# Kernel tuning notes

Hardware: AMD Instinct MI355X
Metric: run time of the kernel (lower is better)

The kernel has to match this reference:

```python
import jax, jax.numpy as jnp
import numpy as np

B, S, DIM, LW, CHUNK = 4, 4096, 512, 512, 64


def _l2n(x):
    n = jnp.sqrt(jnp.sum(x * x, axis=-1, keepdims=True))
    return x / jnp.maximum(n, 1e-12)


def setup_inputs() -> dict:
    key = jax.random.key(0)
    k = jax.random.split(key, 10)
    s = 1.0 / np.sqrt(DIM)
    return {
        "x": jax.random.normal(k[0], (B, S, DIM), jnp.float32),
        "Wq": jax.random.normal(k[1], (DIM, DIM), jnp.float32) * s,
        "Wk": jax.random.normal(k[2], (DIM, DIM), jnp.float32) * s,
        "Wv": jax.random.normal(k[3], (DIM, DIM), jnp.float32) * s,
        "init_w1": jax.random.normal(k[4], (LW, DIM), jnp.float32) * 0.02,
        "init_b1": jnp.zeros((LW,), jnp.float32),
        "init_w2": jax.random.normal(k[5], (DIM, LW), jnp.float32) * 0.02,
        "init_b2": jnp.zeros((DIM,), jnp.float32),
        "alpha_w": jax.random.normal(k[6], (DIM,), jnp.float32) * s,
        "alpha_b": jnp.full((1,), -5.0, jnp.float32),
        "eta_w": jax.random.normal(k[7], (DIM,), jnp.float32) * s,
        "eta_b": jnp.full((1,), 2.0, jnp.float32),
        "theta_w": jax.random.normal(k[8], (DIM,), jnp.float32) * s,
        "theta_b": jnp.full((1,), -4.6, jnp.float32),
        "chunk_size": CHUNK,
    }


def reference(x, Wq, Wk, Wv, init_w1, init_b1, init_w2, init_b2,
              alpha_w, alpha_b, eta_w, eta_b, theta_w, theta_b, chunk_size):
    b, s, d = x.shape
    c = int(chunk_size)
    nC = s // c
    lw = init_w1.shape[0]
    # per-sample memory params (broadcast of shared init) + zero momentum
    w1 = jnp.broadcast_to(init_w1, (b, lw, d))
    b1 = jnp.broadcast_to(init_b1, (b, lw))
    w2 = jnp.broadcast_to(init_w2, (b, d, lw))
    b2 = jnp.broadcast_to(init_b2, (b, d))
    mom = (jnp.zeros_like(w1), jnp.zeros_like(b1), jnp.zeros_like(w2), jnp.zeros_like(b2))
    xc = x.reshape(b, nC, c, d).transpose(1, 0, 2, 3)  # [nC, B, C, D]

    def step(carry, x_c):
        (w1, b1, w2, b2), (mw1, mb1, mw2, mb2) = carry
        q = _l2n(x_c @ Wq.T)
        k_ = _l2n(x_c @ Wk.T)
        v = x_c @ Wv.T
        # gates per token -> chunk-averaged, [B]
        a = jax.nn.sigmoid(x_c @ alpha_w + alpha_b).mean(axis=1)
        e = jax.nn.sigmoid(x_c @ eta_w + eta_b).mean(axis=1)
        t = jax.nn.sigmoid(x_c @ theta_w + theta_b).mean(axis=1)
        # retrieval with stale (chunk-constant) memory params
        hq = jax.nn.silu(jnp.einsum('bcd,bhd->bch', q, w1) + b1[:, None, :])
        y = jnp.einsum('bch,bdh->bcd', hq, w2) + b2[:, None, :]
        # per-token grads of mse(mlp(k), v) (mean over feature dim), chunk-averaged.
        # Analytic grads == autodiff of the tiny MLP; avoids [B,C,LW,D] intermediates.
        pre = jnp.einsum('bcd,bhd->bch', k_, w1) + b1[:, None, :]
        sg = jax.nn.sigmoid(pre)
        hk = pre * sg  # silu
        vp = jnp.einsum('bch,bdh->bcd', hk, w2) + b2[:, None, :]
        dvp = 2.0 * (vp - v) / d  # dL/d vp for mse over feature dim
        g_b2 = dvp.mean(axis=1)
        g_w2 = jnp.einsum('bcd,bch->bdh', dvp, hk) / c
        dh = jnp.einsum('bcd,bdh->bch', dvp, w2) * (sg * (1.0 + pre * (1.0 - sg)))
        g_b1 = dh.mean(axis=1)
        g_w1 = jnp.einsum('bch,bcd->bhd', dh, k_) / c
        a3, e3, t3 = a[:, None, None], e[:, None, None], t[:, None, None]
        a2, e2, t2 = a[:, None], e[:, None], t[:, None]
        nmw1 = e3 * mw1 - t3 * g_w1
        nmb1 = e2 * mb1 - t2 * g_b1
        nmw2 = e3 * mw2 - t3 * g_w2
        nmb2 = e2 * mb2 - t2 * g_b2
        nw1 = (1.0 - a3) * w1 + nmw1
        nb1 = (1.0 - a2) * b1 + nmb1
        nw2 = (1.0 - a3) * w2 + nmw2
        nb2 = (1.0 - a2) * b2 + nmb2
        return ((nw1, nb1, nw2, nb2), (nmw1, nmb1, nmw2, nmb2)), y

    _, ys = jax.lax.scan(step, ((w1, b1, w2, b2), mom), xc)
    return ys.transpose(1, 0, 2, 3).reshape(b, s, d)
```

## Files before the change

### kernel.cpp

```cpp
#include <hip/hip_runtime.h>
#include <hip/hip_bf16.h>

#define BB 4
#define SS 4096
#define DD 512
#define LWW 512
#define CC 64
#define NCH 64

typedef unsigned short u16;
using fragAB = __attribute__((ext_vector_type(8))) short;
using fragC  = __attribute__((ext_vector_type(4))) float;
using u16x4  = __attribute__((ext_vector_type(4))) short;

__device__ __forceinline__ short f2bf(float f){
  unsigned u = __float_as_uint(f);
  u = (u + 0x7FFFu + ((u >> 16) & 1u)) >> 16;
  return (short)u;
}
__device__ __forceinline__ float bf2f(short s){
  return __uint_as_float(((unsigned)(u16)s) << 16);
}
__device__ __forceinline__ fragC zeroC(){ fragC z = {0.f,0.f,0.f,0.f}; return z; }

__device__ __forceinline__ fragAB frag_bf16g(const u16* __restrict__ base, int ld, int r0, int k0, int lane){
  return *(const fragAB*)(base + (size_t)(r0 + (lane & 15)) * ld + k0 + ((lane >> 4) << 3));
}
__device__ __forceinline__ fragAB frag_lds(const short* base, int ld, int r0, int k0, int lane){
  return *(const fragAB*)(base + (r0 + (lane & 15)) * ld + k0 + ((lane >> 4) << 3));
}
#define MFMA16(a,b,c) __builtin_amdgcn_mfma_f32_16x16x32_bf16(a,b,c,0,0,0)

__device__ __forceinline__ void ld_sys(fragAB& r, const u16* p){
  asm volatile("global_load_dwordx4 %0, %1, off sc0 sc1" : "=v"(r) : "v"(p) : "memory");
}
__device__ __forceinline__ void st_sys8(u16* p, u16x4 v){
  asm volatile("global_store_dwordx2 %0, %1, off sc0 sc1" :: "v"(p), "v"(v) : "memory");
}
__device__ __forceinline__ void st_sys16(u16* p, fragAB v){
  asm volatile("global_store_dwordx4 %0, %1, off sc0 sc1" :: "v"(p), "v"(v) : "memory");
}
#define WAITVM(N) do { asm volatile("s_waitcnt vmcnt(" #N ")" ::: "memory"); \
                       __builtin_amdgcn_sched_barrier(0); } while (0)

__device__ __forceinline__ const u16* taddr(const u16* base, int c, int kq){
  return base + (((size_t)((kq >> 4)*64 + c)) << 4) + (kq & 15);
}

__device__ __forceinline__ void bar_sync(unsigned* slots, unsigned phase, int tl){
  asm volatile("s_waitcnt vmcnt(0)" ::: "memory");
  __builtin_amdgcn_sched_barrier(0);
  __syncthreads();
  if (threadIdx.x == 0)
    __hip_atomic_store(slots + (size_t)tl*32, phase, __ATOMIC_RELAXED, __HIP_MEMORY_SCOPE_AGENT);
  if (threadIdx.x < 64){
    bool mine = threadIdx.x < 32;
    unsigned* sp = slots + (size_t)(threadIdx.x & 31)*32;
    for (;;){
      unsigned v = mine ? __hip_atomic_load(sp, __ATOMIC_RELAXED, __HIP_MEMORY_SCOPE_AGENT) : phase;
      if (__all((int)(v >= phase))) break;
      __builtin_amdgcn_s_sleep(1);
    }
  }
  __syncthreads();
}

__global__ __launch_bounds__(256) void k_cvt(const float* __restrict__ x,
    const float* __restrict__ Wq, const float* __restrict__ Wk, const float* __restrict__ Wv,
    u16* __restrict__ xb, u16* __restrict__ Wc, unsigned* __restrict__ bar){
  size_t i = (size_t)blockIdx.x * 256 + threadIdx.x;
  if (blockIdx.x == 0){
    for (int z = threadIdx.x; z < 4096; z += 256) bar[z] = 0u;
  }
  const size_t NX4 = (size_t)BB*SS*DD/4;
  const size_t NW4 = (size_t)DD*DD/4;
  if (i < NX4){
    float4 v = ((const float4*)x)[i];
    u16x4 o = { f2bf(v.x), f2bf(v.y), f2bf(v.z), f2bf(v.w) };
    *(u16x4*)(xb + 4*i) = o;
  } else if (i < NX4 + 3*NW4){
    size_t j = i - NX4;
    const float* src = (j < NW4) ? Wq : (j < 2*NW4) ? Wk : Wv;
    size_t jj = j % NW4;
    float4 v = ((const float4*)src)[jj];
    u16x4 o = { f2bf(v.x), f2bf(v.y), f2bf(v.z), f2bf(v.w) };
    *(u16x4*)(Wc + 4*j) = o;
  }
}

__global__ __launch_bounds__(256) void k_proj(const u16* __restrict__ xb,
    const u16* __restrict__ Wc,
    u16* __restrict__ Qb, u16* __restrict__ Kb, float* __restrict__ V){
  int mt = blockIdx.x / 12, nt = blockIdx.x % 12;
  int lane = threadIdx.x & 63, wid = threadIdx.x >> 6;
  int m0 = mt * 64 + wid * 16;
  const u16* Bp = Wc + (size_t)nt * 128 * DD;
  fragC acc[8];
#pragma unroll
  for (int i = 0; i < 8; ++i) acc[i] = zeroC();
  for (int k0 = 0; k0 < DD; k0 += 32){
    fragAB a = frag_bf16g(xb, DD, m0, k0, lane);
#pragma unroll
    for (int nf = 0; nf < 8; ++nf)
      acc[nf] = MFMA16(a, frag_bf16g(Bp, DD, nf*16, k0, lane), acc[nf]);
  }
#pragma unroll
  for (int nf = 0; nf < 8; ++nf){
#pragma unroll
    for (int r = 0; r < 4; ++r){
      int m = m0 + ((lane >> 4) << 2) + r;
      int col = nt*128 + nf*16 + (lane & 15);
      float v = acc[nf][r];
      if (nt < 4)      Qb[(size_t)m*DD + col]        = (u16)f2bf(v);
      else if (nt < 8) Kb[(size_t)m*DD + col - 512]  = (u16)f2bf(v);
      else             V [(size_t)m*DD + col - 1024] = v;
    }
  }
}

__global__ __launch_bounds__(256) void k_norm(u16* __restrict__ Qb, u16* __restrict__ Kb){
  int idx = blockIdx.x * 4 + (threadIdx.x >> 6);
  int lane = threadIdx.x & 63;
  u16* p = (idx < BB*SS ? Qb + (size_t)idx * DD
                        : Kb + (size_t)(idx - BB*SS) * DD) + lane * 8;
  fragAB v = *(const fragAB*)p;
  float f[8]; float s = 0.f;
#pragma unroll
  for (int i = 0; i < 8; ++i){ f[i] = bf2f(v[i]); s += f[i]*f[i]; }
#pragma unroll
  for (int o = 32; o > 0; o >>= 1) s += __shfl_xor(s, o, 64);
  float inv = 1.f / fmaxf(sqrtf(s), 1e-12f);
  fragAB o8;
#pragma unroll
  for (int i = 0; i < 8; ++i) o8[i] = f2bf(f[i] * inv);
  *(fragAB*)p = o8;
}

__global__ __launch_bounds__(256) void k_trans(const u16* __restrict__ Kb, u16* __restrict__ KT){
  __shared__ short tile[64][68];
  int blk = blockIdx.x;
  int b = blk >> 9, rem = blk & 511;
  int st = rem >> 3, dt = rem & 7;
  int s0 = st*64, d0 = dt*64;
  int sr = threadIdx.x & 63, q = threadIdx.x >> 6;
  const u16* src = Kb + ((size_t)b*SS + s0 + sr)*DD + d0 + q*16;
  fragAB v0 = *(const fragAB*)src;
  fragAB v1 = *(const fragAB*)(src + 8);
#pragma unroll
  for (int i = 0; i < 8; ++i){ tile[sr][q*16+i] = v0[i]; tile[sr][q*16+8+i] = v1[i]; }
  __syncthreads();
  fragAB o0, o1;
#pragma unroll
  for (int i = 0; i < 8; ++i){ o0[i] = tile[q*16+i][sr]; o1[i] = tile[q*16+8+i][sr]; }
  u16* dst = KT + ((size_t)b*DD + d0 + sr)*SS + s0 + q*16;
  *(fragAB*)dst = o0;
  *(fragAB*)(dst + 8) = o1;
}

__global__ __launch_bounds__(256) void k_gates(const float* __restrict__ x,
    const float* __restrict__ aw, const float* __restrict__ ab,
    const float* __restrict__ ew, const float* __restrict__ eb,
    const float* __restrict__ tw, const float* __restrict__ tb,
    float* __restrict__ aet){
  __shared__ float part[64][4][3];
  __shared__ float rowsig[64][3];
  int b = blockIdx.x >> 6, t = blockIdx.x & 63;
  int tid = threadIdx.x;
  int r = tid >> 2, p = tid & 3;
  const float4* xp = (const float4*)(x + ((size_t)b*SS + (size_t)t*CC + r) * DD + p * 128);
  const float4* a4 = (const float4*)(aw + p*128);
  const float4* e4 = (const float4*)(ew + p*128);
  const float4* t4 = (const float4*)(tw + p*128);
  float s0 = 0.f, s1 = 0.f, s2 = 0.f;
  for (int i = 0; i < 32; ++i){
    float4 xv = xp[i], av = a4[i], ev = e4[i], tv = t4[i];
    s0 += xv.x*av.x + xv.y*av.y + xv.z*av.z + xv.w*av.w;
    s1 += xv.x*ev.x + xv.y*ev.y + xv.z*ev.z + xv.w*ev.w;
    s2 += xv.x*tv.x + xv.y*tv.y + xv.z*tv.z + xv.w*tv.w;
  }
  part[r][p][0] = s0; part[r][p][1] = s1; part[r][p][2] = s2;
  __syncthreads();
  if (tid < 64){
    float a_ = part[tid][0][0]+part[tid][1][0]+part[tid][2][0]+part[tid][3][0] + ab[0];
    float e_ = part[tid][0][1]+part[tid][1][1]+part[tid][2][1]+part[tid][3][1] + eb[0];
    float t_ = part[tid][0][2]+part[tid][1][2]+part[tid][2][2]+part[tid][3][2] + tb[0];
    rowsig[tid][0] = 1.f/(1.f+expf(-a_));
    rowsig[tid][1] = 1.f/(1.f+expf(-e_));
    rowsig[tid][2] = 1.f/(1.f+expf(-t_));
  }
  __syncthreads();
  if (tid < 3){
    float s = 0.f;
    for (int i = 0; i < 64; ++i) s += rowsig[i][tid];
    aet[((size_t)b*NCH + t)*3 + tid] = s * (1.f/64.f);
  }
}

__global__ __launch_bounds__(512, 2) void k_scan(
    const u16* __restrict__ Qb, const u16* __restrict__ Kb, const u16* __restrict__ KTg,
    const float* __restrict__ V, const float* __restrict__ aet,
    const float* __restrict__ iw1, const float* __restrict__ ib1,
    const float* __restrict__ iw2, const float* __restrict__ ib2,
    u16* __restrict__ hkb, u16* __restrict__ hqs, u16* __restrict__ hkT,
    u16* __restrict__ dvpb, u16* __restrict__ w2Tb,
    float* __restrict__ out, unsigned* __restrict__ barb)
{
  __shared__ __align__(16) short s_w1[16*520];
  __shared__ __align__(16) short s_w2[16*520];
  __shared__ __align__(16) short s_pf[16*520];
  __shared__ __align__(16) short s_t[16*72];
  __shared__ __align__(16) short s_hk[64*16];
  __shared__ __align__(16) short s_hq[64*16];
  __shared__ float s_part[64][17];
  __shared__ float s_b1[16], s_mb1[16], s_b2[16], s_mb2[16];

  const int tid  = threadIdx.x;
  const int lane = tid & 63;
  const int wid  = tid >> 6;
  const int q    = lane >> 4;
  const int l15  = lane & 15;
  const int qk   = q << 3;
  const int b    = (blockIdx.x & 7) >> 1;
  const int tl   = ((blockIdx.x >> 3) << 1) | (blockIdx.x & 1);
  const int h0   = tl * 16;
  const int d0   = tl * 16;
  unsigned* slots = barb + (size_t)b * 1024;
  unsigned  ph   = 0;

  const u16* Kball = Kb  + (size_t)b*SS*DD;
  const u16* Qball = Qb  + (size_t)b*SS*DD;
  const u16* KTbat = KTg + (size_t)b*DD*SS;
  u16* hk_b  = hkb  + (size_t)b*CC*LWW;
  u16* hq_b  = hqs  + (size_t)b*CC*LWW;
  u16* hkT_b = hkT  + (size_t)b*LWW*CC;
  u16* dv_b  = dvpb + (size_t)b*CC*DD;
  const size_t W2TBUF = (size_t)BB*DD*LWW;

  float w1f[16], mw1f[16], w2f[16], mw2f[16], actr[4];

  {
    u16* w2T0 = w2Tb + (size_t)b*DD*LWW;
#pragma unroll
    for (int nf = 0; nf < 4; ++nf){
      u16x4 pk;
#pragma unroll
      for (int r = 0; r < 4; ++r){
        int hr = q*4 + r;
        int dcol = wid*64 + nf*16 + l15;
        float a = iw1[(size_t)(h0 + hr)*DD + dcol];
        w1f[nf*4+r] = a; mw1f[nf*4+r] = 0.f;
        s_w1[hr*520 + dcol] = f2bf(a);
        float c = iw2[(size_t)(d0 + hr)*LWW + dcol];
        w2f[nf*4+r] = c; mw2f[nf*4+r] = 0.f;
        s_w2[hr*520 + dcol] = f2bf(c);
        pk[r] = f2bf(c);
      }
      st_sys8(w2T0 + (size_t)(wid*64 + nf*16 + l15)*DD + d0 + q*4, pk);
    }
    if (tid < 16){
      s_b1[tid] = ib1[h0 + tid]; s_mb1[tid] = 0.f;
      s_b2[tid] = ib2[d0 + tid]; s_mb2[tid] = 0.f;
    }
#pragma unroll
    for (int r = 0; r < 4; ++r) actr[r] = 0.f;
    WAITVM(0);
    __syncthreads();
  }

  for (int t = 0; t < NCH; ++t){
    if (t > 0){
      fragAB kfr[8];
      {
        const u16* KTm = KTbat + (size_t)(t-1)*CC;
#pragma unroll
        for (int nf = 0; nf < 4; ++nf)
#pragma unroll
          for (int kk = 0; kk < 2; ++kk)
            kfr[nf*2+kk] = frag_bf16g(KTm, SS, wid*64 + nf*16, kk*32, lane);
      }
      {
        const int cst = (wid & 3) * 16;
        const int kh  = (wid >> 2) * 256;
        fragAB fa[8];
        fragC a0 = zeroC();
#pragma unroll
        for (int j = 0; j < 8; ++j) ld_sys(fa[j], taddr(dv_b, cst + l15, kh + j*32 + qk));
        WAITVM(4);
#pragma unroll
        for (int j = 0; j < 4; ++j) a0 = MFMA16(fa[j], frag_lds(s_pf, 520, 0, kh + j*32, lane), a0);
        WAITVM(0);
#pragma unroll
        for (int j = 4; j < 8; ++j) a0 = MFMA16(fa[j], frag_lds(s_pf, 520, 0, kh + j*32, lane), a0);
        if (wid >= 4){
#pragma unroll
          for (int r = 0; r < 4; ++r) s_part[cst + q*4 + r][l15] = a0[r];
        }
        __syncthreads();
        if (wid < 4){
#pragma unroll
          for (int r = 0; r < 4; ++r){
            float v = (a0[r] + s_part[cst + q*4 + r][l15]) * actr[r];
            s_t[l15*72 + cst + q*4 + r] = f2bf(v);
          }
        }
      }
      __syncthreads();
      {
        fragC ag[4];
#pragma unroll
        for (int i = 0; i < 4; ++i) ag[i] = zeroC();
#pragma unroll
        for (int kk = 0; kk < 2; ++kk){
          fragAB af = frag_lds(s_t, 72, 0, kk*32, lane);
#pragma unroll
          for (int nf = 0; nf < 4; ++nf)
            ag[nf] = MFMA16(af, kfr[nf*2+kk], ag[nf]);
        }
        const float* g3 = aet + ((size_t)b*NCH + (t-1)) * 3;
        float ga = g3[0], ge = g3[1], gth = g3[2];
#pragma unroll
        for (int nf = 0; nf < 4; ++nf)
#pragma unroll
          for (int r = 0; r < 4; ++r){
            float g  = ag[nf][r] * (1.f/64.f);
            float m_ = ge*mw1f[nf*4+r] - gth*g;
            float w_ = (1.f-ga)*w1f[nf*4+r] + m_;
            mw1f[nf*4+r] = m_; w1f[nf*4+r] = w_;
            s_w1[(q*4+r)*520 + wid*64 + nf*16 + l15] = f2bf(w_);
          }
        if (tid < 16){
          const fragAB* row = (const fragAB*)(s_t + tid*72);
          float s = 0.f;
#pragma unroll
          for (int j = 0; j < 8; ++j){
            fragAB v = row[j];
#pragma unroll
            for (int i = 0; i < 8; ++i) s += bf2f(v[i]);
          }
          float gb = s * (1.f/64.f);
          float m_ = ge*s_mb1[tid] - gth*gb;
          float bn = (1.f-ga)*s_b1[tid] + m_;
          s_mb1[tid] = m_; s_b1[tid] = bn;
        }
      }
    }
    __syncthreads();
    {
      const u16* Ac = (wid < 4 ? Kball : Qball) + (size_t)t*CC*DD;
      int m0 = (wid & 3) * 16;
      fragC acc = zeroC();
      for (int k0 = 0; k0 < DD; k0 += 32)
        acc = MFMA16(frag_bf16g(Ac, DD, m0, k0, lane),
                     frag_lds(s_w1, 520, 0, k0, lane), acc);
      float bb = s_b1[l15];
      if (wid < 4){
        u16x4 pk;
#pragma unroll
        for (int r = 0; r < 4; ++r){
          int c = m0 + q*4 + r;
          float pre = acc[r] + bb;
          float sg  = 1.f/(1.f+expf(-pre));
          float hkv = pre * sg;
          actr[r]   = sg * (1.f + pre * (1.f - sg));
          short hb  = f2bf(hkv);
          s_hk[c*16 + l15] = hb;
          pk[r] = hb;
        }
        st_sys8(hkT_b + (size_t)(h0 + l15)*CC + m0 + q*4, pk);
      } else {
#pragma unroll
        for (int r = 0; r < 4; ++r){
          int c = m0 + q*4 + r;
          float hqv = acc[r] + bb;
          float s2  = 1.f/(1.f+expf(-hqv));
          s_hq[c*16 + l15] = f2bf(hqv * s2);
        }
      }
    }
    __syncthreads();
    if (tid < 128){
      st_sys16(hk_b + (size_t)tl*1024 + tid*8, *(const fragAB*)(s_hk + tid*8));
    } else if (tid < 256){
      int i = tid - 128;
      st_sys16(hq_b + (size_t)tl*1024 + i*8, *(const fragAB*)(s_hq + i*8));
    }
    ph++; bar_sync(slots, ph, tl);

    {
      const u16* Ah = (wid < 4) ? hq_b : hk_b;
      int m0 = (wid & 3) * 16;
      fragC acc = zeroC();
      fragAB va[4], vb[4], hfr[8];
      float vv[4];
      if (wid >= 4){
#pragma unroll
        for (int r = 0; r < 4; ++r)
          vv[r] = V[((size_t)b*SS + (size_t)t*CC + m0 + q*4 + r)*DD + d0 + l15];
      }
#pragma unroll
      for (int j = 0; j < 4; ++j) ld_sys(va[j], taddr(Ah, m0 + l15, j*32 + qk));
#pragma unroll
      for (int j = 0; j < 4; ++j) ld_sys(vb[j], taddr(Ah, m0 + l15, 128 + j*32 + qk));
      WAITVM(4);
#pragma unroll
      for (int j = 0; j < 4; ++j) acc = MFMA16(va[j], frag_lds(s_w2, 520, 0, j*32, lane), acc);
#pragma unroll
      for (int j = 0; j < 4; ++j) ld_sys(va[j], taddr(Ah, m0 + l15, 256 + j*32 + qk));
      WAITVM(4);
#pragma unroll
      for (int j = 0; j < 4; ++j) acc = MFMA16(vb[j], frag_lds(s_w2, 520, 0, 128 + j*32, lane), acc);
#pragma unroll
      for (int j = 0; j < 4; ++j) ld_sys(vb[j], taddr(Ah, m0 + l15, 384 + j*32 + qk));
      WAITVM(4);
#pragma unroll
      for (int j = 0; j < 4; ++j) acc = MFMA16(va[j], frag_lds(s_w2, 520, 0, 256 + j*32, lane), acc);
#pragma unroll
      for (int nf = 0; nf < 4; ++nf)
#pragma unroll
        for (int kk = 0; kk < 2; ++kk)
          ld_sys(hfr[nf*2+kk], hkT_b + (size_t)(wid*64 + nf*16 + l15)*CC + kk*32 + qk);
      WAITVM(8);
#pragma unroll
      for (int j = 0; j < 4; ++j) acc = MFMA16(vb[j], frag_lds(s_w2, 520, 0, 384 + j*32, lane), acc);

      float bb = s_b2[l15];
      if (wid < 4){
#pragma unroll
        for (int r = 0; r < 4; ++r){
          int c = m0 + q*4 + r;
          __builtin_nontemporal_store(acc[r] + bb,
            &out[((size_t)b*SS + (size_t)t*CC + c)*DD + d0 + l15]);
        }
      } else {
#pragma unroll
        for (int r = 0; r < 4; ++r){
          int c = m0 + q*4 + r;
          float dvv = (acc[r] + bb - vv[r]) * (2.f/512.f);
          short db_ = f2bf(dvv);
          s_hk[c*16 + l15] = db_;
          s_t[l15*72 + c]  = db_;
        }
      }
      __syncthreads();
      if (wid < 4) { WAITVM(4); } else { WAITVM(0); }
      if (tid < 128)
        st_sys16(dv_b + (size_t)tl*1024 + tid*8, *(const fragAB*)(s_hk + tid*8));
      {
        fragC ag[4];
#pragma unroll
        for (int i = 0; i < 4; ++i) ag[i] = zeroC();
#pragma unroll
        for (int kk = 0; kk < 2; ++kk){
          fragAB af = frag_lds(s_t, 72, 0, kk*32, lane);
#pragma unroll
          for (int nf = 0; nf < 4; ++nf)
            ag[nf] = MFMA16(af, hfr[nf*2+kk], ag[nf]);
        }
        fragAB t0, t1;
        int hr = tid >> 5;
        int c0 = (tid & 31) << 4;
        if (t + 1 < NCH){
          const u16* w2Tp = w2Tb + (size_t)(t&1)*W2TBUF + (size_t)b*DD*LWW;
          const u16* src = w2Tp + (size_t)(h0 + hr)*DD + c0;
          ld_sys(t0, src);
          ld_sys(t1, src + 8);
        }
        const float* g3 = aet + ((size_t)b*NCH + t) * 3;
        float ga = g3[0], ge = g3[1], gth = g3[2];
        u16* w2Tn = w2Tb + (size_t)((t+1)&1)*W2TBUF + (size_t)b*DD*LWW;
#pragma unroll
        for (int nf = 0; nf < 4; ++nf){
          u16x4 pk;
#pragma unroll
          for (int r = 0; r < 4; ++r){
            float g  = ag[nf][r] * (1.f/64.f);
            float m_ = ge*mw2f[nf*4+r] - gth*g;
            float w_ = (1.f-ga)*w2f[nf*4+r] + m_;
            mw2f[nf*4+r] = m_; w2f[nf*4+r] = w_;
            short wb = f2bf(w_);
            s_w2[(q*4+r)*520 + wid*64 + nf*16 + l15] = wb;
            pk[r] = wb;
          }
          st_sys8(w2Tn + (size_t)(wid*64 + nf*16 + l15)*DD + d0 + q*4, pk);
        }
        if (tid < 16){
          const fragAB* row = (const fragAB*)(s_t + tid*72);
          float s = 0.f;
#pragma unroll
          for (int j = 0; j < 8; ++j){
            fragAB v = row[j];
#pragma unroll
            for (int i = 0; i < 8; ++i) s += bf2f(v[i]);
          }
          float gb = s * (1.f/64.f);
          float m_ = ge*s_mb2[tid] - gth*gb;
          float bn = (1.f-ga)*s_b2[tid] + m_;
          s_mb2[tid] = m_; s_b2[tid] = bn;
        }
        if (t + 1 < NCH){
          WAITVM(0);
          *(fragAB*)(s_pf + hr*520 + c0)     = t0;
          *(fragAB*)(s_pf + hr*520 + c0 + 8) = t1;
        }
      }
    }
    ph++; bar_sync(slots, ph, tl);
  }
}

extern "C" void kernel_launch(void* const* d_in, const int* in_sizes, int n_in,
                              void* d_out, int out_size, void* d_ws, size_t ws_size,
                              hipStream_t stream){
  const float* x   = (const float*)d_in[0];
  const float* Wq  = (const float*)d_in[1];
  const float* Wk  = (const float*)d_in[2];
  const float* Wv  = (const float*)d_in[3];
  const float* iw1 = (const float*)d_in[4];
  const float* ib1 = (const float*)d_in[5];
  const float* iw2 = (const float*)d_in[6];
  const float* ib2 = (const float*)d_in[7];
  const float* aw  = (const float*)d_in[8];
  const float* ab  = (const float*)d_in[9];
  const float* ew  = (const float*)d_in[10];
  const float* eb  = (const float*)d_in[11];
  const float* tw  = (const float*)d_in[12];
  const float* tb  = (const float*)d_in[13];
  float* out = (float*)d_out;

  float* fw = (float*)d_ws;
  float* V    = fw;  fw += (size_t)BB*SS*DD;
  float* aet  = fw;  fw += (size_t)BB*NCH*3 + 64;
  unsigned* bar = (unsigned*)fw; fw += 4096;
  u16* xb   = (u16*)fw;
  u16* Wc   = xb   + (size_t)BB*SS*DD;
  u16* Qb   = Wc   + (size_t)3*DD*DD;
  u16* Kb   = Qb   + (size_t)BB*SS*DD;
  u16* hkb  = Kb   + (size_t)BB*SS*DD;
  u16* hqs  = hkb  + (size_t)BB*CC*LWW;
  u16* hkT  = hqs  + (size_t)BB*CC*LWW;
  u16* dvpb = hkT  + (size_t)BB*LWW*CC;
  u16* w2Tb = dvpb + (size_t)BB*CC*DD;
  u16* KTg  = xb;

  k_cvt  <<<8960, 256, 0, stream>>>(x, Wq, Wk, Wv, xb, Wc, bar);
  k_proj <<<3072, 256, 0, stream>>>(xb, Wc, Qb, Kb, V);
  k_norm <<<8192, 256, 0, stream>>>(Qb, Kb);
  k_trans<<<2048, 256, 0, stream>>>(Kb, KTg);
  k_gates<<<256,  256, 0, stream>>>(x, aw, ab, ew, eb, tw, tb, aet);
  k_scan <<<128,  512, 0, stream>>>(Qb, Kb, KTg, V, aet, iw1, ib1, iw2, ib2,
                                    hkb, hqs, hkT, dvpb, w2Tb, out, bar);
}
```

Measured before the change: 1.438 ms.

## Replace transposed w2 exchange with redundant column-slice w2 update and split barriers

Each block now keeps its own transposed column slice of w2 in registers and LDS, and updates it locally from an exchanged transposed dvp and a locally stored hk transpose. This replaces writing the full transposed w2 to global memory and reloading it every chunk. The grid barrier is split into arrive and wait halves so the redundant w2c update overlaps barrier latency. The cost is extra MFMA work, registers and LDS per block, plus extra dvT global stores.

Measured after the change: 1.756 ms. 1.22x slower.

```diff
diff --git a/kernel.cpp b/kernel.cpp
--- a/kernel.cpp
+++ b/kernel.cpp
@@ -47,12 +47,14 @@
   return base + (((size_t)((kq >> 4)*64 + c)) << 4) + (kq & 15);
 }
 
-__device__ __forceinline__ void bar_sync(unsigned* slots, unsigned phase, int tl){
+__device__ __forceinline__ void bar_arrive(unsigned* slots, unsigned phase, int tl){
   asm volatile("s_waitcnt vmcnt(0)" ::: "memory");
   __builtin_amdgcn_sched_barrier(0);
   __syncthreads();
   if (threadIdx.x == 0)
     __hip_atomic_store(slots + (size_t)tl*32, phase, __ATOMIC_RELAXED, __HIP_MEMORY_SCOPE_AGENT);
+}
+__device__ __forceinline__ void bar_wait(unsigned* slots, unsigned phase){
   if (threadIdx.x < 64){
     bool mine = threadIdx.x < 32;
     unsigned* sp = slots + (size_t)(threadIdx.x & 31)*32;
@@ -202,13 +204,14 @@
     const float* __restrict__ iw1, const float* __restrict__ ib1,
     const float* __restrict__ iw2, const float* __restrict__ ib2,
     u16* __restrict__ hkb, u16* __restrict__ hqs, u16* __restrict__ hkT,
-    u16* __restrict__ dvpb, u16* __restrict__ w2Tb,
+    u16* __restrict__ dvpb, u16* __restrict__ dvTg,
     float* __restrict__ out, unsigned* __restrict__ barb)
 {
   __shared__ __align__(16) short s_w1[16*520];
   __shared__ __align__(16) short s_w2[16*520];
-  __shared__ __align__(16) short s_pf[16*520];
+  __shared__ __align__(16) short s_w2c[16*520];
   __shared__ __align__(16) short s_t[16*72];
+  __shared__ __align__(16) short s_hkTb[2][16*72];
   __shared__ __align__(16) short s_hk[64*16];
   __shared__ __align__(16) short s_hq[64*16];
   __shared__ float s_part[64][17];
@@ -234,15 +237,13 @@
   u16* hq_b  = hqs  + (size_t)b*CC*LWW;
   u16* hkT_b = hkT  + (size_t)b*LWW*CC;
   u16* dv_b  = dvpb + (size_t)b*CC*DD;
-  const size_t W2TBUF = (size_t)BB*DD*LWW;
-
-  float w1f[16], mw1f[16], w2f[16], mw2f[16], actr[4];
+  u16* dvT_b = dvTg + (size_t)b*DD*CC;
+
+  float w1f[16], mw1f[16], w2f[16], mw2f[16], w2cf[16], mw2cf[16], actr[4];
 
   {
-    u16* w2T0 = w2Tb + (size_t)b*DD*LWW;
 #pragma unroll
     for (int nf = 0; nf < 4; ++nf){
-      u16x4 pk;
 #pragma unroll
       for (int r = 0; r < 4; ++r){
         int hr = q*4 + r;
@@ -253,9 +254,10 @@
         float c = iw2[(size_t)(d0 + hr)*LWW + dcol];
         w2f[nf*4+r] = c; mw2f[nf*4+r] = 0.f;
         s_w2[hr*520 + dcol] = f2bf(c);
-        pk[r] = f2bf(c);
-      }
-      st_sys8(w2T0 + (size_t)(wid*64 + nf*16 + l15)*DD + d0 + q*4, pk);
+        float c2 = iw2[(size_t)dcol*LWW + (h0 + hr)];
+        w2cf[nf*4+r] = c2; mw2cf[nf*4+r] = 0.f;
+        s_w2c[hr*520 + dcol] = f2bf(c2);
+      }
     }
     if (tid < 16){
       s_b1[tid] = ib1[h0 + tid]; s_mb1[tid] = 0.f;
@@ -263,11 +265,11 @@
     }
 #pragma unroll
     for (int r = 0; r < 4; ++r) actr[r] = 0.f;
-    WAITVM(0);
     __syncthreads();
   }
 
   for (int t = 0; t < NCH; ++t){
+    fragAB dfr[8];
     if (t > 0){
       fragAB kfr[8];
       {
@@ -287,10 +289,10 @@
         for (int j = 0; j < 8; ++j) ld_sys(fa[j], taddr(dv_b, cst + l15, kh + j*32 + qk));
         WAITVM(4);
 #pragma unroll
-        for (int j = 0; j < 4; ++j) a0 = MFMA16(fa[j], frag_lds(s_pf, 520, 0, kh + j*32, lane), a0);
+        for (int j = 0; j < 4; ++j) a0 = MFMA16(fa[j], frag_lds(s_w2c, 520, 0, kh + j*32, lane), a0);
         WAITVM(0);
 #pragma unroll
-        for (int j = 4; j < 8; ++j) a0 = MFMA16(fa[j], frag_lds(s_pf, 520, 0, kh + j*32, lane), a0);
+        for (int j = 4; j < 8; ++j) a0 = MFMA16(fa[j], frag_lds(s_w2c, 520, 0, kh + j*32, lane), a0);
         if (wid >= 4){
 #pragma unroll
           for (int r = 0; r < 4; ++r) s_part[cst + q*4 + r][l15] = a0[r];
@@ -355,6 +357,7 @@
       float bb = s_b1[l15];
       if (wid < 4){
         u16x4 pk;
+        short* hT = &s_hkTb[t & 1][0];
 #pragma unroll
         for (int r = 0; r < 4; ++r){
           int c = m0 + q*4 + r;
@@ -364,6 +367,7 @@
           actr[r]   = sg * (1.f + pre * (1.f - sg));
           short hb  = f2bf(hkv);
           s_hk[c*16 + l15] = hb;
+          hT[l15*72 + c]   = hb;
           pk[r] = hb;
         }
         st_sys8(hkT_b + (size_t)(h0 + l15)*CC + m0 + q*4, pk);
@@ -384,7 +388,40 @@
       int i = tid - 128;
       st_sys16(hq_b + (size_t)tl*1024 + i*8, *(const fragAB*)(s_hq + i*8));
     }
-    ph++; bar_sync(slots, ph, tl);
+    if (t > 0){
+#pragma unroll
+      for (int nf = 0; nf < 4; ++nf)
+#pragma unroll
+        for (int kk = 0; kk < 2; ++kk)
+          ld_sys(dfr[nf*2+kk], dvT_b + (size_t)(wid*64 + nf*16 + l15)*CC + kk*32 + qk);
+    }
+    ph++; bar_arrive(slots, ph, tl);
+    if (t > 0){
+      fragC ag2[4];
+#pragma unroll
+      for (int i = 0; i < 4; ++i) ag2[i] = zeroC();
+      const short* hTp = &s_hkTb[(t-1) & 1][0];
+#pragma unroll
+      for (int kk = 0; kk < 2; ++kk){
+        fragAB af2 = frag_lds(hTp, 72, 0, kk*32, lane);
+#pragma unroll
+        for (int nf = 0; nf < 4; ++nf)
+          ag2[nf] = MFMA16(af2, dfr[nf*2+kk], ag2[nf]);
+      }
+      const float* g3 = aet + ((size_t)b*NCH + (t-1)) * 3;
+      float ga = g3[0], ge = g3[1], gth = g3[2];
+#pragma unroll
+      for (int nf = 0; nf < 4; ++nf)
+#pragma unroll
+        for (int r = 0; r < 4; ++r){
+          float g  = ag2[nf][r] * (1.f/64.f);
+          float m_ = ge*mw2cf[nf*4+r] - gth*g;
+          float w_ = (1.f-ga)*w2cf[nf*4+r] + m_;
+          mw2cf[nf*4+r] = m_; w2cf[nf*4+r] = w_;
+          s_w2c[(q*4+r)*520 + wid*64 + nf*16 + l15] = f2bf(w_);
+        }
+    }
+    bar_wait(slots, ph);
 
     {
       const u16* Ah = (wid < 4) ? hq_b : hk_b;
@@ -442,9 +479,14 @@
         }
       }
       __syncthreads();
-      if (wid < 4) { WAITVM(4); } else { WAITVM(0); }
-      if (tid < 128)
+      if (tid < 128){
         st_sys16(dv_b + (size_t)tl*1024 + tid*8, *(const fragAB*)(s_hk + tid*8));
+      } else if (tid < 256){
+        int i = tid - 128;
+        int row = i >> 3, seg = i & 7;
+        st_sys16(dvT_b + (size_t)(d0 + row)*CC + seg*8, *(const fragAB*)(s_t + row*72 + seg*8));
+      }
+      ph++; bar_arrive(slots, ph, tl);
       {
         fragC ag[4];
 #pragma unroll
@@ -456,33 +498,18 @@
           for (int nf = 0; nf < 4; ++nf)
             ag[nf] = MFMA16(af, hfr[nf*2+kk], ag[nf]);
         }
-        fragAB t0, t1;
-        int hr = tid >> 5;
-        int c0 = (tid & 31) << 4;
-        if (t + 1 < NCH){
-          const u16* w2Tp = w2Tb + (size_t)(t&1)*W2TBUF + (size_t)b*DD*LWW;
-          const u16* src = w2Tp + (size_t)(h0 + hr)*DD + c0;
-          ld_sys(t0, src);
-          ld_sys(t1, src + 8);
-        }
         const float* g3 = aet + ((size_t)b*NCH + t) * 3;
         float ga = g3[0], ge = g3[1], gth = g3[2];
-        u16* w2Tn = w2Tb + (size_t)((t+1)&1)*W2TBUF + (size_t)b*DD*LWW;
-#pragma unroll
-        for (int nf = 0; nf < 4; ++nf){
-          u16x4 pk;
+#pragma unroll
+        for (int nf = 0; nf < 4; ++nf)
 #pragma unroll
           for (int r = 0; r < 4; ++r){
             float g  = ag[nf][r] * (1.f/64.f);
             float m_ = ge*mw2f[nf*4+r] - gth*g;
             float w_ = (1.f-ga)*w2f[nf*4+r] + m_;
             mw2f[nf*4+r] = m_; w2f[nf*4+r] = w_;
-            short wb = f2bf(w_);
-            s_w2[(q*4+r)*520 + wid*64 + nf*16 + l15] = wb;
-            pk[r] = wb;
+            s_w2[(q*4+r)*520 + wid*64 + nf*16 + l15] = f2bf(w_);
           }
-          st_sys8(w2Tn + (size_t)(wid*64 + nf*16 + l15)*DD + d0 + q*4, pk);
-        }
         if (tid < 16){
           const fragAB* row = (const fragAB*)(s_t + tid*72);
           float s = 0.f;
@@ -497,14 +524,9 @@
           float bn = (1.f-ga)*s_b2[tid] + m_;
           s_mb2[tid] = m_; s_b2[tid] = bn;
         }
-        if (t + 1 < NCH){
-          WAITVM(0);
-          *(fragAB*)(s_pf + hr*520 + c0)     = t0;
-          *(fragAB*)(s_pf + hr*520 + c0 + 8) = t1;
-        }
-      }
-    }
-    ph++; bar_sync(slots, ph, tl);
+      }
+      bar_wait(slots, ph);
+    }
   }
 }
 
@@ -539,7 +561,7 @@
   u16* hqs  = hkb  + (size_t)BB*CC*LWW;
   u16* hkT  = hqs  + (size_t)BB*CC*LWW;
   u16* dvpb = hkT  + (size_t)BB*LWW*CC;
-  u16* w2Tb = dvpb + (size_t)BB*CC*DD;
+  u16* dvTg = dvpb + (size_t)BB*CC*DD;
   u16* KTg  = xb;
 
   k_cvt  <<<8960, 256, 0, stream>>>(x, Wq, Wk, Wv, xb, Wc, bar);
@@ -548,5 +570,5 @@
   k_trans<<<2048, 256, 0, stream>>>(Kb, KTg);
   k_gates<<<256,  256, 0, stream>>>(x, aw, ab, ew, eb, tw, tb, aet);
   k_scan <<<128,  512, 0, stream>>>(Qb, Kb, KTg, V, aet, iw1, ib1, iw2, ib2,
-                                    hkb, hqs, hkT, dvpb, w2Tb, out, bar);
-}
+                                    hkb, hqs, hkT, dvpb, dvTg, out, bar);
+}
```
